# Performance work log

Hardware: AMD Instinct MI355X
Metric: run time of the kernel (lower is better)

Reference implementation:

```python
import jax, jax.numpy as jnp
import numpy as np

B, C, H, W = 32, 384, 32, 32
NH = 4            # num_heads
CC = 192          # conv_channels = ceil(384/2)
HID = 1536        # mlp hidden = 4*dim
EPS = 1e-6


def _ln2d(x, w, b):
    # LayerNorm over channel axis of NCHW
    u = x.mean(1, keepdims=True)
    s = ((x - u) ** 2).mean(1, keepdims=True)
    return w[:, None, None] * ((x - u) * jax.lax.rsqrt(s + EPS)) + b[:, None, None]


def setup_inputs() -> dict:
    key = jax.random.key(0)
    ks = jax.random.split(key, 8)
    f = lambda k, shp, sc: jax.random.normal(k, shp, jnp.float32) * sc
    return {
        "x": f(ks[0], (B, C, H, W), 1.0),
        "conv_w": f(ks[1], (CC, 1, 3, 3), 0.1),
        "conv_b": jnp.zeros((CC,), jnp.float32),
        "nxca_w": jnp.ones((C,), jnp.float32),
        "nxca_b": jnp.zeros((C,), jnp.float32),
        "temp": jnp.ones((NH, 1, 1), jnp.float32),
        "qkv_w": f(ks[2], (3 * C, C), 0.05),
        "qkv_b": jnp.zeros((3 * C,), jnp.float32),
        "proj_w": f(ks[3], (C, C), 0.05),
        "proj_b": jnp.zeros((C,), jnp.float32),
        "norm_w": jnp.ones((C,), jnp.float32),
        "norm_b": jnp.zeros((C,), jnp.float32),
        "fc1_w": f(ks[4], (HID, C), 0.05),
        "fc1_b": jnp.zeros((HID,), jnp.float32),
        "fc2_w": f(ks[5], (C, HID), 0.05),
        "fc2_b": jnp.zeros((C,), jnp.float32),
        "gamma_xca": jnp.ones((C,), jnp.float32),
        "gamma": jnp.ones((C,), jnp.float32),
    }


def reference(x, conv_w, conv_b, nxca_w, nxca_b, temp, qkv_w, qkv_b,
              proj_w, proj_b, norm_w, norm_b, fc1_w, fc1_b, fc2_w, fc2_b,
              gamma_xca, gamma):
    b, c, h, w = x.shape
    n = h * w
    hd = c // NH
    # depthwise 3x3 conv on first CC channels (in-place in torch -> shortcut
    # taken AFTER the conv, faithfully reproduced here)
    xc = jax.lax.conv_general_dilated(
        x[:, :CC], conv_w, (1, 1), ((1, 1), (1, 1)), feature_group_count=CC
    ) + conv_b[None, :, None, None]
    x = jnp.concatenate([xc, x[:, CC:]], axis=1)
    shortcut = x
    # XCA branch
    y = _ln2d(x, nxca_w, nxca_b)
    yf = y.reshape(b, c, n).transpose(0, 2, 1)                       # [B,N,C]
    qkv = (yf @ qkv_w.T + qkv_b).reshape(b, n, 3, NH, hd).transpose(2, 0, 3, 1, 4)
    q, k, v = qkv[0], qkv[1], qkv[2]                                  # [B,h,N,hd]
    q = q / jnp.maximum(jnp.linalg.norm(q, axis=-1, keepdims=True), 1e-12)
    k = k / jnp.maximum(jnp.linalg.norm(k, axis=-1, keepdims=True), 1e-12)
    attn = jax.nn.softmax(jnp.einsum('bhnd,bhmd->bhnm', q, k) * temp, axis=-1)
    o = jnp.einsum('bhnm,bhmd->bhnd', attn, v).transpose(0, 2, 1, 3).reshape(b, n, c)
    o = (o @ proj_w.T + proj_b).transpose(0, 2, 1).reshape(b, c, h, w)
    x = shortcut + gamma_xca[None, :, None, None] * o
    # MLP branch
    shortcut2 = x
    z = _ln2d(x, norm_w, norm_b).transpose(0, 2, 3, 1).reshape(b, n, c)
    z = jax.nn.gelu(z @ fc1_w.T + fc1_b, approximate=False) @ fc2_w.T + fc2_b
    z = z.reshape(b, h, w, c).transpose(0, 3, 1, 2)
    return shortcut2 + gamma[None, :, None, None] * z
```

## Files before the change

### kernel.cpp

```cpp
#include <hip/hip_runtime.h>
#include <cstdint>

typedef unsigned short u16;
typedef unsigned int u32;
typedef unsigned long long u64;
typedef __attribute__((ext_vector_type(4))) float f32x4;
typedef __attribute__((ext_vector_type(8))) __bf16 bf16x8;
typedef __attribute__((ext_vector_type(8))) u16 u16x8;

#define DEV __device__ __forceinline__

DEV u16 cvt16(float f) {
  __bf16 h = (__bf16)f;
  return __builtin_bit_cast(u16, h);
}
DEV u16 f2bf(float f) {
  u32 u = __builtin_bit_cast(u32, f);
  u += 0x7fffu + ((u >> 16) & 1u);
  return (u16)(u >> 16);
}
DEV float bflo2f(u32 packed) { return __builtin_bit_cast(float, packed << 16); }
DEV float bfhi2f(u32 packed) { return __builtin_bit_cast(float, packed & 0xffff0000u); }

DEV void g2l16(void* lds_wave_base, const void* gsrc) {
  __builtin_amdgcn_global_load_lds(
      (const __attribute__((address_space(1))) u32*)gsrc,
      (__attribute__((address_space(3))) u32*)lds_wave_base, 16, 0, 0);
}

DEV float gelu_tanh(float v) {
  float z = v * (0.7978845608f + 0.0356774081f * v * v);
  float e = __expf(2.0f * z);
  float th = 1.0f - 2.0f / (e + 1.0f);
  return 0.5f * v * (1.0f + th);
}

__global__ __launch_bounds__(256) void conv_k(const float* __restrict__ x,
                                              const float* __restrict__ cw,
                                              const float* __restrict__ cb,
                                              float* __restrict__ xc) {
  int id = blockIdx.x * 256 + threadIdx.x;
  int p = id & 1023;
  int bc = id >> 10;
  int c = bc % 384;
  float v;
  if (c < 192) {
    int hh = p >> 5, ww = p & 31;
    float a = cb[c];
    const float* xp = x + ((size_t)bc << 10);
    const float* wp = cw + c * 9;
#pragma unroll
    for (int dy = 0; dy < 3; ++dy) {
      int y = hh + dy - 1;
      if ((unsigned)y < 32u) {
#pragma unroll
        for (int dx = 0; dx < 3; ++dx) {
          int xw = ww + dx - 1;
          if ((unsigned)xw < 32u) a += xp[y * 32 + xw] * wp[dy * 3 + dx];
        }
      }
    }
    v = a;
  } else {
    v = x[id];
  }
  xc[id] = v;
}

__global__ __launch_bounds__(256) void cvt_k(const float* __restrict__ in,
                                             u16* __restrict__ out, int n) {
  int id = blockIdx.x * 256 + threadIdx.x;
  if (id < n) out[id] = f2bf(in[id]);
}

__global__ __launch_bounds__(256) void ln_t_k(const float* __restrict__ X,
                                              const float* __restrict__ w,
                                              const float* __restrict__ bsh,
                                              u16* __restrict__ Y) {
  __shared__ float tile[384][33];
  __shared__ float ps[8][32], ps2[8][32];
  __shared__ float mean_s[32], rstd_s[32];
  const int b = blockIdx.y;
  const int p0 = blockIdx.x * 32;
  const int t = threadIdx.x;
  const int pl = t & 31, cg = t >> 5;
  const float* xb = X + (((size_t)b * 384) << 10) + p0 + pl;
  float s = 0.f, s2 = 0.f;
  for (int c = cg; c < 384; c += 8) {
    float v = xb[(size_t)c << 10];
    tile[c][pl] = v;
    s += v;
    s2 += v * v;
  }
  ps[cg][pl] = s;
  ps2[cg][pl] = s2;
  __syncthreads();
  if (t < 32) {
    float a = 0.f, a2 = 0.f;
#pragma unroll
    for (int g = 0; g < 8; ++g) { a += ps[g][t]; a2 += ps2[g][t]; }
    float mu = a * (1.f / 384.f);
    float var = a2 * (1.f / 384.f) - mu * mu;
    mean_s[t] = mu;
    rstd_s[t] = rsqrtf(var + 1e-6f);
  }
  __syncthreads();
  const int cl = t & 63, pg = t >> 6;
  for (int p = pg; p < 32; p += 4) {
    float mu = mean_s[p], rs = rstd_s[p];
    size_t orow = (((size_t)b << 10) + p0 + p) * 384;
#pragma unroll
    for (int cc = 0; cc < 6; ++cc) {
      int c = cc * 64 + cl;
      float v = (tile[c][p] - mu) * rs * w[c] + bsh[c];
      Y[orow + c] = f2bf(v);
    }
  }
}

__global__ __launch_bounds__(256) void normqk_k(u16* __restrict__ Qn,
                                                u16* __restrict__ Kn,
                                                const float* __restrict__ temp) {
  const int t = threadIdx.x;
  const int w = t >> 6, l = t & 63;
  const int rg = l >> 4, li = l & 15;
  const int row = blockIdx.x * 16 + w * 4 + rg;
  const float tmp = temp[(row >> 10) & 3];
#pragma unroll
  for (int arr = 0; arr < 2; ++arr) {
    u16* p = arr ? (Kn + (size_t)row * 128 + li * 6)
                 : (Qn + (size_t)row * 96 + li * 6);
    u32 a = *(const u32*)p;
    u32 b2 = *(const u32*)(p + 2);
    u32 c = *(const u32*)(p + 4);
    float v[6] = {bflo2f(a), bfhi2f(a), bflo2f(b2), bfhi2f(b2), bflo2f(c), bfhi2f(c)};
    float ss = 0.f;
#pragma unroll
    for (int i = 0; i < 6; ++i) ss += v[i] * v[i];
#pragma unroll
    for (int mk = 1; mk < 16; mk <<= 1) ss += __shfl_xor(ss, mk, 64);
    float sc = 1.0f / fmaxf(sqrtf(ss), 1e-12f);
    if (arr == 0) sc *= tmp;
    u32 o0 = (u32)f2bf(v[0] * sc) | ((u32)f2bf(v[1] * sc) << 16);
    u32 o1 = (u32)f2bf(v[2] * sc) | ((u32)f2bf(v[3] * sc) << 16);
    u32 o2 = (u32)f2bf(v[4] * sc) | ((u32)f2bf(v[5] * sc) << 16);
    *(u32*)p = o0;
    *(u32*)(p + 2) = o1;
    *(u32*)(p + 4) = o2;
  }
}

__global__ __launch_bounds__(256) void attn_k(const u16* __restrict__ Qn,
                                              const u16* __restrict__ Kg,
                                              const u16* __restrict__ Vg,
                                              u16* __restrict__ O,
                                              const float* __restrict__ temp) {
  __shared__ u16 Kt[2][8192];
  __shared__ u16 Vt[2][6144];
  __shared__ u16 Pt[4][2304];
  const int t = threadIdx.x;
  const int w = t >> 6, l = t & 63;
  const int l15 = l & 15, kg = l >> 4;
  const int id = blockIdx.x;
  const int xcd = id & 7, jj = id >> 3;
  const int bh = xcd * 16 + (jj >> 3);
  const int qb = jj & 7;
  const int b = bh >> 2, h = bh & 3;
  const int q0 = qb * 128 + w * 32;
  const u16* Qb = Qn + (size_t)bh * 98304;
  const u16* Kbg = Kg + (size_t)bh * 131072;
  const u16* Vbg = Vg + (size_t)bh * 98304;
  const float T = fabsf(temp[h]);

  u32 sK[4], sV[3];
#pragma unroll
  for (int j = 0; j < 4; ++j) {
    u32 s = w * 4096 + j * 1024 + l * 16;
    sK[j] = s ^ (((s >> 8) & 7) << 4);
  }
#pragma unroll
  for (int j = 0; j < 3; ++j) {
    u32 s = w * 3072 + j * 1024 + l * 16;
    u32 u = s ^ (((s >> 7) & 7) << 4);
    sV[j] = (u >> 7) * 2048 + (u & 127);
  }
  u32 cs[3];
#pragma unroll
  for (int kk = 0; kk < 3; ++kk)
    cs[kk] = (u32)((kk * 64 + kg * 16) ^ ((l15 & 7) << 4));

  bf16x8 qf[2][3];
#pragma unroll
  for (int f = 0; f < 2; ++f) {
    const u16* qp = Qb + (size_t)(q0 + f * 16 + l15) * 96 + kg * 8;
#pragma unroll
    for (int kk = 0; kk < 3; ++kk) qf[f][kk] = *(const bf16x8*)(qp + kk * 32);
  }
  f32x4 oa[2][6];
#pragma unroll
  for (int f = 0; f < 2; ++f)
#pragma unroll
    for (int d = 0; d < 6; ++d) oa[f][d] = {0.f, 0.f, 0.f, 0.f};
  float l_r[2][4] = {{0.f, 0.f, 0.f, 0.f}, {0.f, 0.f, 0.f, 0.f}};
  __bf16* Pw = (__bf16*)&Pt[w][0];

#define STAGE(buf, kv0)                                                        \
  {                                                                            \
    const char* kb = (const char*)Kbg + (size_t)(kv0) * 256;                   \
    const char* vb = (const char*)Vbg + (size_t)(kv0) * 2;                     \
    char* kd = (char*)&Kt[buf][0] + w * 4096;                                  \
    char* vd = (char*)&Vt[buf][0] + w * 3072;                                  \
    g2l16(kd, kb + sK[0]);                                                     \
    g2l16(kd + 1024, kb + sK[1]);                                              \
    g2l16(kd + 2048, kb + sK[2]);                                              \
    g2l16(kd + 3072, kb + sK[3]);                                              \
    g2l16(vd, vb + sV[0]);                                                     \
    g2l16(vd + 1024, vb + sV[1]);                                              \
    g2l16(vd + 2048, vb + sV[2]);                                              \
  }

  STAGE(0, 0);
  for (int tt = 0; tt < 16; ++tt) {
    const int cur = tt & 1;
    if (tt < 15) {
      STAGE(cur ^ 1, (tt + 1) * 64);
      asm volatile("s_waitcnt vmcnt(7)" ::: "memory");
    } else {
      asm volatile("s_waitcnt vmcnt(0)" ::: "memory");
    }
    __builtin_amdgcn_s_barrier();
    const char* Kc = (const char*)&Kt[cur][0];
    const char* Vc = (const char*)&Vt[cur][0];
    f32x4 s0[4], s1[4];
#pragma unroll
    for (int n = 0; n < 4; ++n) { s0[n] = {0.f, 0.f, 0.f, 0.f}; s1[n] = {0.f, 0.f, 0.f, 0.f}; }
#pragma unroll
    for (int n = 0; n < 4; ++n) {
      const char* krow = Kc + ((n * 16 + l15) << 8);
#pragma unroll
      for (int kk = 0; kk < 3; ++kk) {
        bf16x8 kf = *(const bf16x8*)(krow + cs[kk]);
        s0[n] = __builtin_amdgcn_mfma_f32_16x16x32_bf16(qf[0][kk], kf, s0[n], 0, 0, 0);
        s1[n] = __builtin_amdgcn_mfma_f32_16x16x32_bf16(qf[1][kk], kf, s1[n], 0, 0, 0);
      }
    }
#pragma unroll
    for (int n = 0; n < 4; ++n) {
#pragma unroll
      for (int j = 0; j < 4; ++j) {
        float p0 = __expf(s0[n][j] - T);
        float p1 = __expf(s1[n][j] - T);
        l_r[0][j] += p0;
        l_r[1][j] += p1;
        Pw[(kg * 4 + j) * 72 + n * 16 + l15] = (__bf16)p0;
        Pw[(16 + kg * 4 + j) * 72 + n * 16 + l15] = (__bf16)p1;
      }
    }
#pragma unroll
    for (int kk = 0; kk < 2; ++kk) {
      bf16x8 pf0 = *(const bf16x8*)(Pw + (size_t)l15 * 72 + kk * 32 + kg * 8);
      bf16x8 pf1 = *(const bf16x8*)(Pw + (size_t)(16 + l15) * 72 + kk * 32 + kg * 8);
#pragma unroll
      for (int d = 0; d < 6; ++d) {
        bf16x8 vf = *(const bf16x8*)(Vc + ((d * 16 + l15) << 7) + cs[kk]);
        oa[0][d] = __builtin_amdgcn_mfma_f32_16x16x32_bf16(pf0, vf, oa[0][d], 0, 0, 0);
        oa[1][d] = __builtin_amdgcn_mfma_f32_16x16x32_bf16(pf1, vf, oa[1][d], 0, 0, 0);
      }
    }
    __builtin_amdgcn_s_barrier();
  }
#undef STAGE
  float inv[2][4];
#pragma unroll
  for (int f = 0; f < 2; ++f)
#pragma unroll
    for (int j = 0; j < 4; ++j) {
      float sum = l_r[f][j];
#pragma unroll
      for (int mk = 1; mk < 16; mk <<= 1) sum += __shfl_xor(sum, mk, 64);
      inv[f][j] = 1.0f / sum;
    }
#pragma unroll
  for (int f = 0; f < 2; ++f)
#pragma unroll
    for (int d = 0; d < 6; ++d)
#pragma unroll
      for (int j = 0; j < 4; ++j) {
        int tok = q0 + f * 16 + kg * 4 + j;
        O[((size_t)b * 1024 + tok) * 384 + h * 96 + d * 16 + l15] =
            f2bf(oa[f][d][j] * inv[f][j]);
      }
}

template <int EPI, int SWZ>
__global__ __launch_bounds__(256) void gemm_k(const u16* __restrict__ A,
                                              const u16* __restrict__ B, int M,
                                              int N, int K,
                                              const float* __restrict__ bias,
                                              const float* gamma,
                                              const float* res, void* outp,
                                              int nbx) {
  __shared__ u16 SM[16384];
  const int t = threadIdx.x;
  const int w = t >> 6, l = t & 63;
  const int l15 = l & 15, kg = l >> 4;
  int bx, by;
  if (SWZ == 1) {
    int id = blockIdx.x;
    int xcd = id & 7, jj = id >> 3;
    int q = jj / nbx;
    bx = jj - q * nbx;
    by = xcd * 32 + q;
  } else if (SWZ == 2) {
    int id = blockIdx.x;
    int xcd = id & 7, jj = id >> 3;
    by = jj % 3;
    bx = (jj / 3) * 8 + xcd;
  } else {
    bx = blockIdx.x; by = blockIdx.y;
  }
  const int m0 = by * 128, n0 = bx * 128;
  const int wr = w >> 1, wc = w & 1;

  const int off1 = w * 1024 + l * 16;
  const int off2 = 4096 + w * 1024 + l * 16;
  const int r1 = off1 >> 6, c1 = off1 & 63;
  const int r2 = off2 >> 6, c2 = off2 & 63;
  const size_t ldab = (size_t)K * 2;
  const char* pa1 = (const char*)A + (size_t)(m0 + r1) * ldab + c1;
  const char* pa2 = (const char*)A + (size_t)(m0 + r2) * ldab + c2;
  const char* pb1 = (const char*)B + (size_t)(n0 + r1) * ldab + c1;
  const char* pb2 = (const char*)B + (size_t)(n0 + r2) * ldab + c2;
  char* SMc = (char*)SM;

  f32x4 acc[4][4];
#pragma unroll
  for (int m = 0; m < 4; ++m)
#pragma unroll
    for (int n = 0; n < 4; ++n) acc[m][n] = {0.f, 0.f, 0.f, 0.f};

  const int nkt = K >> 5;
  {
    char* ad = SMc + w * 1024;
    char* bd = SMc + 16384 + w * 1024;
    g2l16(ad, pa1); g2l16(ad + 4096, pa2);
    g2l16(bd, pb1); g2l16(bd + 4096, pb2);
  }
  __syncthreads();
  for (int kt = 0; kt < nkt; ++kt) {
    const int buf = kt & 1;
    if (kt + 1 < nkt) {
      const size_t o = (size_t)(kt + 1) * 64;
      char* ad = SMc + (buf ^ 1) * 8192 + w * 1024;
      char* bd = SMc + 16384 + (buf ^ 1) * 8192 + w * 1024;
      g2l16(ad, pa1 + o); g2l16(ad + 4096, pa2 + o);
      g2l16(bd, pb1 + o); g2l16(bd + 4096, pb2 + o);
    }
    const u16* Ab = SM + buf * 4096;
    const u16* Bb = SM + 8192 + buf * 4096;
    bf16x8 af[4], bfr[4];
#pragma unroll
    for (int m = 0; m < 4; ++m)
      af[m] = *(const bf16x8*)(Ab + (wr * 64 + m * 16 + l15) * 32 + kg * 8);
#pragma unroll
    for (int n = 0; n < 4; ++n)
      bfr[n] = *(const bf16x8*)(Bb + (wc * 64 + n * 16 + l15) * 32 + kg * 8);
#pragma unroll
    for (int m = 0; m < 4; ++m)
#pragma unroll
      for (int n = 0; n < 4; ++n)
        acc[m][n] = __builtin_amdgcn_mfma_f32_16x16x32_bf16(af[m], bfr[n], acc[m][n], 0, 0, 0);
    __syncthreads();
  }

  if (EPI == 2) {
    float* out = (float*)outp;
#pragma unroll
    for (int m = 0; m < 4; ++m) {
#pragma unroll
      for (int n = 0; n < 4; ++n) {
        int tok = n0 + wc * 64 + n * 16 + l15;
        int bb = tok >> 10, p = tok & 1023;
#pragma unroll
        for (int j = 0; j < 4; ++j) {
          int c = m0 + wr * 64 + m * 16 + kg * 4 + j;
          size_t addr = (((size_t)(bb * 384 + c)) << 10) + p;
          out[addr] = res[addr] + gamma[c] * (acc[m][n][j] + bias[c]);
        }
      }
    }
    return;
  }

  const int sec = (EPI == 3) ? (n0 / 384) : 0;
  if (EPI == 3 && sec == 2) {
    u16* Vp = (u16*)outp + 12582912 + 16777216;
#pragma unroll
    for (int m = 0; m < 4; ++m) {
      const int tokbase = m0 + wr * 64 + m * 16 + kg * 4;
      const int bb = tokbase >> 10, nb = tokbase & 1023;
#pragma unroll
      for (int n = 0; n < 4; ++n) {
        int within = n0 - 768 + wc * 64 + n * 16 + l15;
        int hh = within / 96;
        int dd = within - hh * 96;
        float bs = bias[768 + within];
        int bh = bb * 4 + hh;
        u64 pk = 0;
#pragma unroll
        for (int j = 0; j < 4; ++j)
          pk |= (u64)cvt16(acc[m][n][j] + bs) << (16 * j);
        *(u64*)(Vp + ((size_t)bh * 96 + dd) * 1024 + nb) = pk;
      }
    }
    return;
  }

  {
    u16* Ct = SM;
    float bs[4];
#pragma unroll
    for (int n = 0; n < 4; ++n) bs[n] = bias[n0 + wc * 64 + n * 16 + l15];
    u16* cw_ = Ct + (wr * 64 + kg * 4) * 128 + wc * 64 + l15;
#pragma unroll
    for (int m = 0; m < 4; ++m)
#pragma unroll
      for (int n = 0; n < 4; ++n)
#pragma unroll
        for (int j = 0; j < 4; ++j) {
          float v = acc[m][n][j] + bs[n];
          if (EPI == 1) v = gelu_tanh(v);
          cw_[(m * 16 + j) * 128 + n * 16] = cvt16(v);
        }
    __syncthreads();
    const int row_l = w * 4 + (l >> 4);
    const int colc = (l & 15) * 8;
    const u16* src = Ct + row_l * 128 + colc;
    if (EPI == 1) {
      u16* dst = (u16*)outp + (size_t)(m0 + row_l) * N + n0 + colc;
#pragma unroll
      for (int rr = 0; rr < 8; ++rr)
        *(u16x8*)(dst + (size_t)rr * 16 * N) =
            *(const u16x8*)(src + rr * 16 * 128);
    } else {
      int within = n0 - sec * 384 + colc;
      int hh = within / 96;
      int dd = within - hh * 96;
      int tokb = m0 + row_l;
      int bb = tokb >> 10, nb = tokb & 1023;
      int bh = bb * 4 + hh;
      u16* dp;
      int stride;
      if (sec == 0) {
        dp = (u16*)outp + ((size_t)bh * 1024 + nb) * 96 + dd;
        stride = 16 * 96;
      } else {
        dp = (u16*)outp + 12582912 + (((size_t)bh * 1024 + nb) << 7) + dd;
        stride = 16 * 128;
      }
#pragma unroll
      for (int rr = 0; rr < 8; ++rr) {
        *(u16x8*)dp = *(const u16x8*)(src + rr * 16 * 128);
        dp += stride;
      }
    }
  }
}

extern "C" void kernel_launch(void* const* d_in, const int* in_sizes, int n_in,
                              void* d_out, int out_size, void* d_ws,
                              size_t ws_size, hipStream_t stream) {
  const float* x      = (const float*)d_in[0];
  const float* conv_w = (const float*)d_in[1];
  const float* conv_b = (const float*)d_in[2];
  const float* nxca_w = (const float*)d_in[3];
  const float* nxca_b = (const float*)d_in[4];
  const float* temp   = (const float*)d_in[5];
  const float* qkv_w  = (const float*)d_in[6];
  const float* qkv_b  = (const float*)d_in[7];
  const float* proj_w = (const float*)d_in[8];
  const float* proj_b = (const float*)d_in[9];
  const float* norm_w = (const float*)d_in[10];
  const float* norm_b = (const float*)d_in[11];
  const float* fc1_w  = (const float*)d_in[12];
  const float* fc1_b  = (const float*)d_in[13];
  const float* fc2_w  = (const float*)d_in[14];
  const float* fc2_b  = (const float*)d_in[15];
  const float* g_xca  = (const float*)d_in[16];
  const float* g_mlp  = (const float*)d_in[17];
  (void)in_sizes; (void)n_in; (void)out_size; (void)ws_size;

  char* ws = (char*)d_ws;
  float* xc  = (float*)(ws);
  u16* Y     = (u16*)(ws + 50331648);
  u16* Qn    = (u16*)(ws + 75497472);
  u16* Kn    = (u16*)(ws + 100663296);
  u16* Vt    = (u16*)(ws + 134217728);
  u16* Obuf  = Y;
  u16* H1    = Qn;
  u16* wq    = (u16*)(ws + 176160768);
  u16* wp    = (u16*)(ws + 177045504);
  u16* w1    = (u16*)(ws + 177340416);
  u16* w2    = (u16*)(ws + 178520064);

  cvt_k<<<1728, 256, 0, stream>>>(qkv_w, wq, 442368);
  cvt_k<<<576, 256, 0, stream>>>(proj_w, wp, 147456);
  cvt_k<<<2304, 256, 0, stream>>>(fc1_w, w1, 589824);
  cvt_k<<<2304, 256, 0, stream>>>(fc2_w, w2, 589824);

  conv_k<<<49152, 256, 0, stream>>>(x, conv_w, conv_b, xc);
  ln_t_k<<<dim3(32, 32), 256, 0, stream>>>(xc, nxca_w, nxca_b, Y);
  gemm_k<3, 1><<<2304, 256, 0, stream>>>(Y, wq, 32768, 1152, 384, qkv_b,
                                         nullptr, nullptr, Qn, 9);
  normqk_k<<<8192, 256, 0, stream>>>(Qn, Kn, temp);
  attn_k<<<1024, 256, 0, stream>>>(Qn, Kn, Vt, Obuf, temp);
  gemm_k<2, 2><<<768, 256, 0, stream>>>(wp, Obuf, 384, 32768, 384,
                                        proj_b, g_xca, xc, xc, 0);
  ln_t_k<<<dim3(32, 32), 256, 0, stream>>>(xc, norm_w, norm_b, Y);
  gemm_k<1, 1><<<3072, 256, 0, stream>>>(Y, w1, 32768, 1536, 384, fc1_b,
                                         nullptr, nullptr, H1, 12);
  gemm_k<2, 2><<<768, 256, 0, stream>>>(w2, H1, 384, 32768, 1536,
                                        fc2_b, g_mlp, xc, (float*)d_out, 0);
}
```

Before: 453.9 us.

## Merge weight conversions, halve attention KV tile, and use explicit waitcnt barriers in GEMM

Replaces four separate fp32-to-bf16 weight conversion launches with one fused kernel. The attention kernel now stages 32 keys per iteration instead of 64, which halves its LDS footprint and may raise occupancy, at the cost of twice as many barriers. It also changes the V staging layout and adds scheduling barriers. The GEMM drops __syncthreads in favour of explicit vmcnt waits plus s_barrier, so the next tile's loads can stay in flight while the current tile is computed.

```diff
diff --git a/kernel.cpp b/kernel.cpp
--- a/kernel.cpp
+++ b/kernel.cpp
@@ -67,10 +67,19 @@
   xc[id] = v;
 }
 
-__global__ __launch_bounds__(256) void cvt_k(const float* __restrict__ in,
-                                             u16* __restrict__ out, int n) {
+__global__ __launch_bounds__(256) void cvt4_k(const float* __restrict__ s0,
+                                              const float* __restrict__ s1,
+                                              const float* __restrict__ s2,
+                                              const float* __restrict__ s3,
+                                              u16* __restrict__ d0,
+                                              u16* __restrict__ d1,
+                                              u16* __restrict__ d2,
+                                              u16* __restrict__ d3) {
   int id = blockIdx.x * 256 + threadIdx.x;
-  if (id < n) out[id] = f2bf(in[id]);
+  if (id < 442368) d0[id] = f2bf(s0[id]);
+  else if (id < 589824) d1[id - 442368] = f2bf(s1[id - 442368]);
+  else if (id < 1179648) d2[id - 589824] = f2bf(s2[id - 589824]);
+  else if (id < 1769472) d3[id - 1179648] = f2bf(s3[id - 1179648]);
 }
 
 __global__ __launch_bounds__(256) void ln_t_k(const float* __restrict__ X,
@@ -155,9 +164,9 @@
                                               const u16* __restrict__ Vg,
                                               u16* __restrict__ O,
                                               const float* __restrict__ temp) {
-  __shared__ u16 Kt[2][8192];
-  __shared__ u16 Vt[2][6144];
-  __shared__ u16 Pt[4][2304];
+  __shared__ u16 Kt[2][4096];
+  __shared__ u16 Vt[2][3072];
+  __shared__ u16 Pt[4][1280];
   const int t = threadIdx.x;
   const int w = t >> 6, l = t & 63;
   const int l15 = l & 15, kg = l >> 4;
@@ -172,17 +181,17 @@
   const u16* Vbg = Vg + (size_t)bh * 98304;
   const float T = fabsf(temp[h]);
 
-  u32 sK[4], sV[3];
-#pragma unroll
-  for (int j = 0; j < 4; ++j) {
-    u32 s = w * 4096 + j * 1024 + l * 16;
+  u32 sK[2], sV[2];
+#pragma unroll
+  for (int j = 0; j < 2; ++j) {
+    u32 s = w * 2048 + j * 1024 + l * 16;
     sK[j] = s ^ (((s >> 8) & 7) << 4);
   }
-#pragma unroll
-  for (int j = 0; j < 3; ++j) {
-    u32 s = w * 3072 + j * 1024 + l * 16;
-    u32 u = s ^ (((s >> 7) & 7) << 4);
-    sV[j] = (u >> 7) * 2048 + (u & 127);
+  const int wv = (w < 2) ? w : 2;
+#pragma unroll
+  for (int j = 0; j < 2; ++j) {
+    u32 s = wv * 2048 + j * 1024 + l * 16;
+    sV[j] = (s >> 6) * 2048 + (s & 63);
   }
   u32 cs[3];
 #pragma unroll
@@ -208,34 +217,32 @@
   {                                                                            \
     const char* kb = (const char*)Kbg + (size_t)(kv0) * 256;                   \
     const char* vb = (const char*)Vbg + (size_t)(kv0) * 2;                     \
-    char* kd = (char*)&Kt[buf][0] + w * 4096;                                  \
-    char* vd = (char*)&Vt[buf][0] + w * 3072;                                  \
+    char* kd = (char*)&Kt[buf][0] + w * 2048;                                  \
+    char* vd = (char*)&Vt[buf][0] + wv * 2048;                                 \
     g2l16(kd, kb + sK[0]);                                                     \
     g2l16(kd + 1024, kb + sK[1]);                                              \
-    g2l16(kd + 2048, kb + sK[2]);                                              \
-    g2l16(kd + 3072, kb + sK[3]);                                              \
     g2l16(vd, vb + sV[0]);                                                     \
     g2l16(vd + 1024, vb + sV[1]);                                              \
-    g2l16(vd + 2048, vb + sV[2]);                                              \
   }
 
   STAGE(0, 0);
-  for (int tt = 0; tt < 16; ++tt) {
+  for (int tt = 0; tt < 32; ++tt) {
     const int cur = tt & 1;
-    if (tt < 15) {
-      STAGE(cur ^ 1, (tt + 1) * 64);
-      asm volatile("s_waitcnt vmcnt(7)" ::: "memory");
+    if (tt < 31) {
+      STAGE(cur ^ 1, (tt + 1) * 32);
+      asm volatile("s_waitcnt vmcnt(4)" ::: "memory");
     } else {
       asm volatile("s_waitcnt vmcnt(0)" ::: "memory");
     }
     __builtin_amdgcn_s_barrier();
+    __builtin_amdgcn_sched_barrier(0);
     const char* Kc = (const char*)&Kt[cur][0];
     const char* Vc = (const char*)&Vt[cur][0];
-    f32x4 s0[4], s1[4];
-#pragma unroll
-    for (int n = 0; n < 4; ++n) { s0[n] = {0.f, 0.f, 0.f, 0.f}; s1[n] = {0.f, 0.f, 0.f, 0.f}; }
-#pragma unroll
-    for (int n = 0; n < 4; ++n) {
+    f32x4 s0[2], s1[2];
+#pragma unroll
+    for (int n = 0; n < 2; ++n) { s0[n] = {0.f, 0.f, 0.f, 0.f}; s1[n] = {0.f, 0.f, 0.f, 0.f}; }
+#pragma unroll
+    for (int n = 0; n < 2; ++n) {
       const char* krow = Kc + ((n * 16 + l15) << 8);
 #pragma unroll
       for (int kk = 0; kk < 3; ++kk) {
@@ -245,28 +252,28 @@
       }
     }
 #pragma unroll
-    for (int n = 0; n < 4; ++n) {
+    for (int n = 0; n < 2; ++n) {
 #pragma unroll
       for (int j = 0; j < 4; ++j) {
         float p0 = __expf(s0[n][j] - T);
         float p1 = __expf(s1[n][j] - T);
         l_r[0][j] += p0;
         l_r[1][j] += p1;
-        Pw[(kg * 4 + j) * 72 + n * 16 + l15] = (__bf16)p0;
-        Pw[(16 + kg * 4 + j) * 72 + n * 16 + l15] = (__bf16)p1;
-      }
-    }
-#pragma unroll
-    for (int kk = 0; kk < 2; ++kk) {
-      bf16x8 pf0 = *(const bf16x8*)(Pw + (size_t)l15 * 72 + kk * 32 + kg * 8);
-      bf16x8 pf1 = *(const bf16x8*)(Pw + (size_t)(16 + l15) * 72 + kk * 32 + kg * 8);
+        Pw[(kg * 4 + j) * 40 + n * 16 + l15] = (__bf16)p0;
+        Pw[(16 + kg * 4 + j) * 40 + n * 16 + l15] = (__bf16)p1;
+      }
+    }
+    {
+      bf16x8 pf0 = *(const bf16x8*)(Pw + (size_t)l15 * 40 + kg * 8);
+      bf16x8 pf1 = *(const bf16x8*)(Pw + (size_t)(16 + l15) * 40 + kg * 8);
 #pragma unroll
       for (int d = 0; d < 6; ++d) {
-        bf16x8 vf = *(const bf16x8*)(Vc + ((d * 16 + l15) << 7) + cs[kk]);
+        bf16x8 vf = *(const bf16x8*)(Vc + ((d * 16 + l15) << 6) + kg * 16);
         oa[0][d] = __builtin_amdgcn_mfma_f32_16x16x32_bf16(pf0, vf, oa[0][d], 0, 0, 0);
         oa[1][d] = __builtin_amdgcn_mfma_f32_16x16x32_bf16(pf1, vf, oa[1][d], 0, 0, 0);
       }
     }
+    __builtin_amdgcn_sched_barrier(0);
     __builtin_amdgcn_s_barrier();
   }
 #undef STAGE
@@ -346,7 +353,6 @@
     g2l16(ad, pa1); g2l16(ad + 4096, pa2);
     g2l16(bd, pb1); g2l16(bd + 4096, pb2);
   }
-  __syncthreads();
   for (int kt = 0; kt < nkt; ++kt) {
     const int buf = kt & 1;
     if (kt + 1 < nkt) {
@@ -355,7 +361,12 @@
       char* bd = SMc + 16384 + (buf ^ 1) * 8192 + w * 1024;
       g2l16(ad, pa1 + o); g2l16(ad + 4096, pa2 + o);
       g2l16(bd, pb1 + o); g2l16(bd + 4096, pb2 + o);
-    }
+      asm volatile("s_waitcnt vmcnt(4)" ::: "memory");
+    } else {
+      asm volatile("s_waitcnt vmcnt(0)" ::: "memory");
+    }
+    __builtin_amdgcn_s_barrier();
+    __builtin_amdgcn_sched_barrier(0);
     const u16* Ab = SM + buf * 4096;
     const u16* Bb = SM + 8192 + buf * 4096;
     bf16x8 af[4], bfr[4];
@@ -370,7 +381,8 @@
 #pragma unroll
       for (int n = 0; n < 4; ++n)
         acc[m][n] = __builtin_amdgcn_mfma_f32_16x16x32_bf16(af[m], bfr[n], acc[m][n], 0, 0, 0);
-    __syncthreads();
+    __builtin_amdgcn_sched_barrier(0);
+    __builtin_amdgcn_s_barrier();
   }
 
   if (EPI == 2) {
@@ -503,10 +515,7 @@
   u16* w1    = (u16*)(ws + 177340416);
   u16* w2    = (u16*)(ws + 178520064);
 
-  cvt_k<<<1728, 256, 0, stream>>>(qkv_w, wq, 442368);
-  cvt_k<<<576, 256, 0, stream>>>(proj_w, wp, 147456);
-  cvt_k<<<2304, 256, 0, stream>>>(fc1_w, w1, 589824);
-  cvt_k<<<2304, 256, 0, stream>>>(fc2_w, w2, 589824);
+  cvt4_k<<<6912, 256, 0, stream>>>(qkv_w, proj_w, fc1_w, fc2_w, wq, wp, w1, w2);
 
   conv_k<<<49152, 256, 0, stream>>>(x, conv_w, conv_b, xc);
   ln_t_k<<<dim3(32, 32), 256, 0, stream>>>(xc, nxca_w, nxca_b, Y);
```

After: 452.5 us. No clear change (-0.3%).

## Store QKV token-major, vectorize conv, merge weight casts, loosen GEMM barriers

Applied to the files above, without the earlier changes.

The QKV GEMM now writes Q and K in plain token-major [tokens,1152] layout instead of scattering them into per-head buffers. normqk and attention read that layout directly, with the K staging addresses remapped into the 2304-byte row stride. The depthwise conv computes four outputs per thread using vector loads. The four weight-cast launches are merged into one kernel. The GEMM main loop replaces __syncthreads with explicit vmcnt waits plus s_barrier, so the next tile's loads can stay in flight. These changes target strided scatter writes, launch overhead and barrier stalls, at the cost of strided K/Q reads in attention and the risk of getting the hand-written wait counts wrong.

```diff
diff --git a/kernel.cpp b/kernel.cpp
--- a/kernel.cpp
+++ b/kernel.cpp
@@ -39,38 +39,51 @@
                                               const float* __restrict__ cw,
                                               const float* __restrict__ cb,
                                               float* __restrict__ xc) {
+  const int bc = blockIdx.x;
+  const int c = bc % 384;
+  const int p4 = threadIdx.x * 4;
+  const float* xp = x + ((size_t)bc << 10);
+  float* op = xc + ((size_t)bc << 10) + p4;
+  if (c >= 192) {
+    *(f32x4*)op = *(const f32x4*)(xp + p4);
+    return;
+  }
+  const int hh = p4 >> 5, ww0 = p4 & 31;
+  const float* wb = cw + c * 9;
+  float b0 = cb[c];
+  float a0 = b0, a1 = b0, a2 = b0, a3 = b0;
+#pragma unroll
+  for (int dy = 0; dy < 3; ++dy) {
+    int y = hh + dy - 1;
+    if ((unsigned)y < 32u) {
+      const float* rp = xp + y * 32 + ww0;
+      f32x4 m = *(const f32x4*)rp;
+      float lft = (ww0 > 0) ? rp[-1] : 0.f;
+      float rgt = (ww0 < 28) ? rp[4] : 0.f;
+      float w0 = wb[dy * 3], w1 = wb[dy * 3 + 1], w2 = wb[dy * 3 + 2];
+      a0 += lft * w0 + m[0] * w1 + m[1] * w2;
+      a1 += m[0] * w0 + m[1] * w1 + m[2] * w2;
+      a2 += m[1] * w0 + m[2] * w1 + m[3] * w2;
+      a3 += m[2] * w0 + m[3] * w1 + rgt * w2;
+    }
+  }
+  f32x4 r = {a0, a1, a2, a3};
+  *(f32x4*)op = r;
+}
+
+__global__ __launch_bounds__(256) void cvt4_k(const float* __restrict__ s0,
+                                              const float* __restrict__ s1,
+                                              const float* __restrict__ s2,
+                                              const float* __restrict__ s3,
+                                              u16* __restrict__ d0,
+                                              u16* __restrict__ d1,
+                                              u16* __restrict__ d2,
+                                              u16* __restrict__ d3) {
   int id = blockIdx.x * 256 + threadIdx.x;
-  int p = id & 1023;
-  int bc = id >> 10;
-  int c = bc % 384;
-  float v;
-  if (c < 192) {
-    int hh = p >> 5, ww = p & 31;
-    float a = cb[c];
-    const float* xp = x + ((size_t)bc << 10);
-    const float* wp = cw + c * 9;
-#pragma unroll
-    for (int dy = 0; dy < 3; ++dy) {
-      int y = hh + dy - 1;
-      if ((unsigned)y < 32u) {
-#pragma unroll
-        for (int dx = 0; dx < 3; ++dx) {
-          int xw = ww + dx - 1;
-          if ((unsigned)xw < 32u) a += xp[y * 32 + xw] * wp[dy * 3 + dx];
-        }
-      }
-    }
-    v = a;
-  } else {
-    v = x[id];
-  }
-  xc[id] = v;
-}
-
-__global__ __launch_bounds__(256) void cvt_k(const float* __restrict__ in,
-                                             u16* __restrict__ out, int n) {
-  int id = blockIdx.x * 256 + threadIdx.x;
-  if (id < n) out[id] = f2bf(in[id]);
+  if (id < 442368) d0[id] = f2bf(s0[id]);
+  else if (id < 589824) d1[id - 442368] = f2bf(s1[id - 442368]);
+  else if (id < 1179648) d2[id - 589824] = f2bf(s2[id - 589824]);
+  else if (id < 1769472) d3[id - 1179648] = f2bf(s3[id - 1179648]);
 }
 
 __global__ __launch_bounds__(256) void ln_t_k(const float* __restrict__ X,
@@ -118,18 +131,17 @@
   }
 }
 
-__global__ __launch_bounds__(256) void normqk_k(u16* __restrict__ Qn,
-                                                u16* __restrict__ Kn,
+__global__ __launch_bounds__(256) void normqk_k(u16* __restrict__ QKV,
                                                 const float* __restrict__ temp) {
   const int t = threadIdx.x;
   const int w = t >> 6, l = t & 63;
   const int rg = l >> 4, li = l & 15;
-  const int row = blockIdx.x * 16 + w * 4 + rg;
-  const float tmp = temp[(row >> 10) & 3];
-#pragma unroll
-  for (int arr = 0; arr < 2; ++arr) {
-    u16* p = arr ? (Kn + (size_t)row * 128 + li * 6)
-                 : (Qn + (size_t)row * 96 + li * 6);
+  const int tok = blockIdx.x * 16 + w * 4 + rg;
+  u16* rowp = QKV + (size_t)tok * 1152;
+#pragma unroll
+  for (int seg = 0; seg < 8; ++seg) {
+    const int h = seg & 3, isK = seg >> 2;
+    u16* p = rowp + isK * 384 + h * 96 + li * 6;
     u32 a = *(const u32*)p;
     u32 b2 = *(const u32*)(p + 2);
     u32 c = *(const u32*)(p + 4);
@@ -140,7 +152,7 @@
 #pragma unroll
     for (int mk = 1; mk < 16; mk <<= 1) ss += __shfl_xor(ss, mk, 64);
     float sc = 1.0f / fmaxf(sqrtf(ss), 1e-12f);
-    if (arr == 0) sc *= tmp;
+    if (!isK) sc *= temp[h];
     u32 o0 = (u32)f2bf(v[0] * sc) | ((u32)f2bf(v[1] * sc) << 16);
     u32 o1 = (u32)f2bf(v[2] * sc) | ((u32)f2bf(v[3] * sc) << 16);
     u32 o2 = (u32)f2bf(v[4] * sc) | ((u32)f2bf(v[5] * sc) << 16);
@@ -150,8 +162,7 @@
   }
 }
 
-__global__ __launch_bounds__(256) void attn_k(const u16* __restrict__ Qn,
-                                              const u16* __restrict__ Kg,
+__global__ __launch_bounds__(256) void attn_k(const u16* __restrict__ QKV,
                                               const u16* __restrict__ Vg,
                                               u16* __restrict__ O,
                                               const float* __restrict__ temp) {
@@ -167,8 +178,8 @@
   const int qb = jj & 7;
   const int b = bh >> 2, h = bh & 3;
   const int q0 = qb * 128 + w * 32;
-  const u16* Qb = Qn + (size_t)bh * 98304;
-  const u16* Kbg = Kg + (size_t)bh * 131072;
+  const u16* Qb = QKV + (size_t)b * 1024 * 1152;
+  const char* Kbg = (const char*)QKV + (size_t)b * 1024 * 2304 + 768 + 192 * h;
   const u16* Vbg = Vg + (size_t)bh * 98304;
   const float T = fabsf(temp[h]);
 
@@ -176,7 +187,9 @@
 #pragma unroll
   for (int j = 0; j < 4; ++j) {
     u32 s = w * 4096 + j * 1024 + l * 16;
-    sK[j] = s ^ (((s >> 8) & 7) << 4);
+    u32 row = s >> 8, rem = s & 255;
+    u32 X = rem ^ ((row & 7) << 4);
+    sK[j] = (X < 192) ? (row * 2304 + X) : 0u;
   }
 #pragma unroll
   for (int j = 0; j < 3; ++j) {
@@ -192,7 +205,7 @@
   bf16x8 qf[2][3];
 #pragma unroll
   for (int f = 0; f < 2; ++f) {
-    const u16* qp = Qb + (size_t)(q0 + f * 16 + l15) * 96 + kg * 8;
+    const u16* qp = Qb + (size_t)(q0 + f * 16 + l15) * 1152 + h * 96 + kg * 8;
 #pragma unroll
     for (int kk = 0; kk < 3; ++kk) qf[f][kk] = *(const bf16x8*)(qp + kk * 32);
   }
@@ -206,7 +219,7 @@
 
 #define STAGE(buf, kv0)                                                        \
   {                                                                            \
-    const char* kb = (const char*)Kbg + (size_t)(kv0) * 256;                   \
+    const char* kb = Kbg + (size_t)(kv0) * 2304;                               \
     const char* vb = (const char*)Vbg + (size_t)(kv0) * 2;                     \
     char* kd = (char*)&Kt[buf][0] + w * 4096;                                  \
     char* vd = (char*)&Vt[buf][0] + w * 3072;                                  \
@@ -346,7 +359,6 @@
     g2l16(ad, pa1); g2l16(ad + 4096, pa2);
     g2l16(bd, pb1); g2l16(bd + 4096, pb2);
   }
-  __syncthreads();
   for (int kt = 0; kt < nkt; ++kt) {
     const int buf = kt & 1;
     if (kt + 1 < nkt) {
@@ -355,7 +367,12 @@
       char* bd = SMc + 16384 + (buf ^ 1) * 8192 + w * 1024;
       g2l16(ad, pa1 + o); g2l16(ad + 4096, pa2 + o);
       g2l16(bd, pb1 + o); g2l16(bd + 4096, pb2 + o);
-    }
+      asm volatile("s_waitcnt vmcnt(4)" ::: "memory");
+    } else {
+      asm volatile("s_waitcnt vmcnt(0)" ::: "memory");
+    }
+    __builtin_amdgcn_s_barrier();
+    __builtin_amdgcn_sched_barrier(0);
     const u16* Ab = SM + buf * 4096;
     const u16* Bb = SM + 8192 + buf * 4096;
     bf16x8 af[4], bfr[4];
@@ -370,7 +387,8 @@
 #pragma unroll
       for (int n = 0; n < 4; ++n)
         acc[m][n] = __builtin_amdgcn_mfma_f32_16x16x32_bf16(af[m], bfr[n], acc[m][n], 0, 0, 0);
-    __syncthreads();
+    __builtin_amdgcn_sched_barrier(0);
+    __builtin_amdgcn_s_barrier();
   }
 
   if (EPI == 2) {
@@ -392,9 +410,9 @@
     return;
   }
 
-  const int sec = (EPI == 3) ? (n0 / 384) : 0;
-  if (EPI == 3 && sec == 2) {
-    u16* Vp = (u16*)outp + 12582912 + 16777216;
+  const int sec = (EPI == 4) ? (n0 / 384) : 0;
+  if (EPI == 4 && sec == 2) {
+    u16* Vp = (u16*)(uintptr_t)gamma;
 #pragma unroll
     for (int m = 0; m < 4; ++m) {
       const int tokbase = m0 + wr * 64 + m * 16 + kg * 4;
@@ -443,26 +461,11 @@
         *(u16x8*)(dst + (size_t)rr * 16 * N) =
             *(const u16x8*)(src + rr * 16 * 128);
     } else {
-      int within = n0 - sec * 384 + colc;
-      int hh = within / 96;
-      int dd = within - hh * 96;
-      int tokb = m0 + row_l;
-      int bb = tokb >> 10, nb = tokb & 1023;
-      int bh = bb * 4 + hh;
-      u16* dp;
-      int stride;
-      if (sec == 0) {
-        dp = (u16*)outp + ((size_t)bh * 1024 + nb) * 96 + dd;
-        stride = 16 * 96;
-      } else {
-        dp = (u16*)outp + 12582912 + (((size_t)bh * 1024 + nb) << 7) + dd;
-        stride = 16 * 128;
-      }
-#pragma unroll
-      for (int rr = 0; rr < 8; ++rr) {
-        *(u16x8*)dp = *(const u16x8*)(src + rr * 16 * 128);
-        dp += stride;
-      }
+      u16* dst = (u16*)outp + (size_t)(m0 + row_l) * 1152 + n0 + colc;
+#pragma unroll
+      for (int rr = 0; rr < 8; ++rr)
+        *(u16x8*)(dst + (size_t)rr * 16 * 1152) =
+            *(const u16x8*)(src + rr * 16 * 128);
     }
   }
 }
@@ -493,27 +496,23 @@
   char* ws = (char*)d_ws;
   float* xc  = (float*)(ws);
   u16* Y     = (u16*)(ws + 50331648);
-  u16* Qn    = (u16*)(ws + 75497472);
-  u16* Kn    = (u16*)(ws + 100663296);
-  u16* Vt    = (u16*)(ws + 134217728);
+  u16* QKVr  = (u16*)(ws + 75497472);
+  u16* Vt    = (u16*)(ws + 150994944);
   u16* Obuf  = Y;
-  u16* H1    = Qn;
+  u16* H1    = QKVr;
   u16* wq    = (u16*)(ws + 176160768);
   u16* wp    = (u16*)(ws + 177045504);
   u16* w1    = (u16*)(ws + 177340416);
   u16* w2    = (u16*)(ws + 178520064);
 
-  cvt_k<<<1728, 256, 0, stream>>>(qkv_w, wq, 442368);
-  cvt_k<<<576, 256, 0, stream>>>(proj_w, wp, 147456);
-  cvt_k<<<2304, 256, 0, stream>>>(fc1_w, w1, 589824);
-  cvt_k<<<2304, 256, 0, stream>>>(fc2_w, w2, 589824);
-
-  conv_k<<<49152, 256, 0, stream>>>(x, conv_w, conv_b, xc);
+  cvt4_k<<<6912, 256, 0, stream>>>(qkv_w, proj_w, fc1_w, fc2_w, wq, wp, w1, w2);
+
+  conv_k<<<12288, 256, 0, stream>>>(x, conv_w, conv_b, xc);
   ln_t_k<<<dim3(32, 32), 256, 0, stream>>>(xc, nxca_w, nxca_b, Y);
-  gemm_k<3, 1><<<2304, 256, 0, stream>>>(Y, wq, 32768, 1152, 384, qkv_b,
-                                         nullptr, nullptr, Qn, 9);
-  normqk_k<<<8192, 256, 0, stream>>>(Qn, Kn, temp);
-  attn_k<<<1024, 256, 0, stream>>>(Qn, Kn, Vt, Obuf, temp);
+  gemm_k<4, 1><<<2304, 256, 0, stream>>>(Y, wq, 32768, 1152, 384, qkv_b,
+                                         (const float*)Vt, nullptr, QKVr, 9);
+  normqk_k<<<2048, 256, 0, stream>>>(QKVr, temp);
+  attn_k<<<1024, 256, 0, stream>>>(QKVr, Vt, Obuf, temp);
   gemm_k<2, 2><<<768, 256, 0, stream>>>(wp, Obuf, 384, 32768, 384,
                                         proj_b, g_xca, xc, xc, 0);
   ln_t_k<<<dim3(32, 32), 256, 0, stream>>>(xc, norm_w, norm_b, Y);
```

Measured after the change: 413.2 us. -9.0%, faster.
